# Kernel tuning notes

Hardware: AMD Instinct MI355X
Metric: run time of the kernel (lower is better)

The kernel has to match this reference:

```python
import jax, jax.numpy as jnp
import numpy as np

T, B, IN_S, H, OUT_S = 2048, 4096, 1, 20, 1


def setup_inputs() -> dict:
    key = jax.random.key(0)
    k_u, k_ih, k_hh, k_out = jax.random.split(key, 4)
    s = 1.0 / np.sqrt(H)  # PyTorch-style uniform init scale (values only; math identical)
    return {
        "u": jax.random.normal(k_u, (T, B, IN_S), dtype=jnp.float32),
        "W_ih": jax.random.uniform(k_ih, (4 * H, IN_S), minval=-s, maxval=s, dtype=jnp.float32),
        "W_hh": jax.random.uniform(k_hh, (4 * H, H), minval=-s, maxval=s, dtype=jnp.float32),
        "W_out": jax.random.uniform(k_out, (OUT_S, H), minval=-s, maxval=s, dtype=jnp.float32),
    }


def _lstm(u, W_ih, W_hh):
    # u: [T, B, IN_S]; PyTorch gate order: i, f, g, o. No biases (bias=False).
    Tn, Bn, _ = u.shape
    # Precompute input projections for all timesteps at once: [T, B, 4H]
    x_proj = jnp.einsum("tbi,gi->tbg", u, W_ih)

    def step(carry, xg):
        h, c = carry  # [B, H] each
        gates = xg + h @ W_hh.T  # [B, 4H]
        i, f, g, o = jnp.split(gates, 4, axis=-1)
        i = jax.nn.sigmoid(i)
        f = jax.nn.sigmoid(f)
        g = jnp.tanh(g)
        o = jax.nn.sigmoid(o)
        c = f * c + i * g
        h = o * jnp.tanh(c)
        return (h, c), h

    h0 = jnp.zeros((Bn, W_hh.shape[1]), dtype=u.dtype)
    c0 = jnp.zeros_like(h0)
    (_, _), ys = jax.lax.scan(step, (h0, c0), x_proj)
    return ys  # [T, B, H]


def reference(u, W_ih, W_hh, W_out):
    ys = _lstm(u, W_ih, W_hh)          # [T, B, H]
    return jnp.einsum("tbh,oh->tbo", ys, W_out)  # [T, B, OUT_S]
```

## Files before the change

kernel.cpp:

```cpp
#include <hip/hip_runtime.h>
#include <hip/hip_bf16.h>
#include <math.h>

#define TT 2048
#define BB 4096
#define HH 20

typedef float v2f __attribute__((ext_vector_type(2)));

#define L2E 1.4426950408889634f

__device__ __forceinline__ float rcp_fast(float x)  { return __builtin_amdgcn_rcpf(x); }
__device__ __forceinline__ float exp2_fast(float x) { return __builtin_amdgcn_exp2f(x); }

__device__ __forceinline__ v2f pk_fma(v2f a, v2f b, v2f c) {
    return __builtin_elementwise_fma(a, b, c);
}

__global__ __launch_bounds__(64, 2) void lstm_fused_kernel(
    const float* __restrict__ u,
    const float* __restrict__ W_ih,
    const float* __restrict__ W_hh,
    const float* __restrict__ W_out,
    float* __restrict__ y)
{
    __shared__ __align__(16) float hbuf[4][HH];

    const int lane  = threadIdx.x;
    const int group = lane / HH;
    const int j     = lane - group * HH;
    const bool is_y = (lane >= 2 * HH) && (lane < 2 * HH + 2);
    const int b_real = blockIdx.x * 2 + group;
    const bool active = (group < 2) && (b_real < BB);
    const int b = active ? b_real : 0;

    for (int i = lane; i < 4 * HH; i += 64) ((float*)hbuf)[i] = 0.0f;
    asm volatile("" ::: "memory");

    v2f wg[4][HH / 2];
    const float gsc[4] = {-L2E, -L2E, -2.0f * L2E, -L2E};
    #pragma unroll
    for (int g = 0; g < 4; ++g) {
        #pragma unroll
        for (int m = 0; m < HH / 2; ++m) {
            wg[g][m].x = gsc[g] * W_hh[(g * HH + j) * HH + 2 * m];
            wg[g][m].y = gsc[g] * W_hh[(g * HH + j) * HH + 2 * m + 1];
        }
    }
    v2f wih2[4];
    #pragma unroll
    for (int g = 0; g < 4; ++g) { wih2[g].x = gsc[g] * W_ih[g * HH + j]; wih2[g].y = 0.0f; }

    int bg = group;
    if (lane >= 2 * HH) {
        bg = is_y ? (lane - 2 * HH) : 2;
        if (is_y) {
            #pragma unroll
            for (int m = 0; m < HH / 2; ++m) {
                wg[0][m].x = W_out[2 * m];
                wg[0][m].y = W_out[2 * m + 1];
            }
            wih2[0].x = 0.0f;
        }
    }

    #pragma unroll
    for (int g = 0; g < 4; ++g) {
        #pragma unroll
        for (int m = 0; m < HH / 2; ++m) {
            asm volatile("" : "+v"(wg[g][m].x), "+v"(wg[g][m].y));
        }
        asm volatile("" : "+v"(wih2[g].x));
    }

    const v2f* hs = (const v2f*)(&hbuf[bg][0]);

    float c = 0.0f;
    const float* __restrict__ up = u + b;
    float* yp = y + blockIdx.x * 2 + (lane - 2 * HH);

    float u_cur[8];
    #pragma unroll
    for (int k = 0; k < 8; ++k) u_cur[k] = up[(size_t)k * BB];

    for (int t8 = 0; t8 < TT; t8 += 8) {
        const int tn = (t8 + 8 < TT) ? (t8 + 8) : t8;
        float u_nxt[8];
        #pragma unroll
        for (int k = 0; k < 8; ++k) u_nxt[k] = up[(size_t)(tn + k) * BB];

        float y8[8];

        #pragma unroll
        for (int tt = 0; tt < 8; ++tt) {
            v2f h2[10];
            #pragma unroll
            for (int m = 0; m < 10; ++m) h2[m] = hs[m];

            const float uv = u_cur[tt];
            const v2f uv2 = {uv, uv};
            v2f a0 = wih2[0] * uv2;
            v2f a1 = wih2[1] * uv2;
            v2f a2 = wih2[2] * uv2;
            v2f a3 = wih2[3] * uv2;

            #pragma unroll
            for (int m = 0; m < 10; ++m) {
                v2f hp = h2[m];
                a2 = pk_fma(wg[2][m], hp, a2);
                a1 = pk_fma(wg[1][m], hp, a1);
                a0 = pk_fma(wg[0][m], hp, a0);
                a3 = pk_fma(wg[3][m], hp, a3);
            }
            const float g2 = a2.x + a2.y;
            const float g1 = a1.x + a1.y;
            const float g0 = a0.x + a0.y;
            const float g3 = a3.x + a3.y;
            y8[tt] = g0;

            const float eg = exp2_fast(g2);
            const float ef = exp2_fast(g1);
            const float ei = exp2_fast(g0);
            const float eo = exp2_fast(g3);
            const float pg  = 1.0f + eg;
            const float pf  = 1.0f + ef;
            const float pi_ = 1.0f + ei;
            const float po  = 1.0f + eo;
            const float mg  = 1.0f - eg;

            const float m1  = pg * pi_;
            const float num = fmaf(c, m1, mg * pf);
            const float r   = rcp_fast(pf * m1);
            c = num * r;
            const float kn  = (-2.0f * L2E) * fabsf(num);
            const float ec  = exp2_fast(kn * r);
            const float pc  = 1.0f + ec;
            const float mcs = copysignf(1.0f - ec, num);
            const float h   = mcs * rcp_fast(po * pc);

            hbuf[group][j] = h;
        }

        if (is_y) {
            #pragma unroll
            for (int k = 0; k < 8; ++k) {
                const int idx = t8 - 1 + k;
                if (idx >= 0) yp[(size_t)idx * BB] = y8[k];
            }
        }

        #pragma unroll
        for (int k = 0; k < 8; ++k) u_cur[k] = u_nxt[k];
    }

    {
        v2f ay = {0.0f, 0.0f};
        #pragma unroll
        for (int m = 0; m < 10; ++m) ay = pk_fma(wg[0][m], hs[m], ay);
        if (is_y) yp[(size_t)(TT - 1) * BB] = ay.x + ay.y;
    }
}

extern "C" void kernel_launch(void* const* d_in, const int* in_sizes, int n_in,
                              void* d_out, int out_size, void* d_ws, size_t ws_size,
                              hipStream_t stream) {
    const float* u     = (const float*)d_in[0];
    const float* W_ih  = (const float*)d_in[1];
    const float* W_hh  = (const float*)d_in[2];
    const float* W_out = (const float*)d_in[3];
    float* y = (float*)d_out;

    const int blocks = BB / 2;
    lstm_fused_kernel<<<dim3(blocks), dim3(64), 0, stream>>>(u, W_ih, W_hh, W_out, y);
}
```

Before: 803.9 us.

## Compute two hidden units per lane to pack four batch rows per wave

Each lane now owns two hidden units of one batch element, so a 64-lane wave handles four sequences instead of two and the grid halves. Gate math and the cell update are written on 2-wide vectors, and the hidden state is stored as a pair. Holding twice as many weights in registers forces one wave per SIMD, which trades latency hiding for fewer waves and better lane utilization.

```diff
diff --git a/kernel.cpp b/kernel.cpp
--- a/kernel.cpp
+++ b/kernel.cpp
@@ -16,72 +16,90 @@
 __device__ __forceinline__ v2f pk_fma(v2f a, v2f b, v2f c) {
     return __builtin_elementwise_fma(a, b, c);
 }
+__device__ __forceinline__ v2f exp2v(v2f x) { v2f r; r.x = exp2_fast(x.x); r.y = exp2_fast(x.y); return r; }
+__device__ __forceinline__ v2f rcpv(v2f x)  { v2f r; r.x = rcp_fast(x.x);  r.y = rcp_fast(x.y);  return r; }
+__device__ __forceinline__ v2f absv(v2f x)  { v2f r; r.x = fabsf(x.x);     r.y = fabsf(x.y);     return r; }
+__device__ __forceinline__ v2f csignv(v2f x, v2f s) {
+    v2f r; r.x = copysignf(x.x, s.x); r.y = copysignf(x.y, s.y); return r;
+}
 
-__global__ __launch_bounds__(64, 2) void lstm_fused_kernel(
+__global__ __launch_bounds__(64, 1) void lstm_fused_kernel(
     const float* __restrict__ u,
     const float* __restrict__ W_ih,
     const float* __restrict__ W_hh,
     const float* __restrict__ W_out,
     float* __restrict__ y)
 {
-    __shared__ __align__(16) float hbuf[4][HH];
+    __shared__ __align__(16) float hbuf[128];
 
-    const int lane  = threadIdx.x;
-    const int group = lane / HH;
-    const int j     = lane - group * HH;
-    const bool is_y = (lane >= 2 * HH) && (lane < 2 * HH + 2);
-    const int b_real = blockIdx.x * 2 + group;
-    const bool active = (group < 2) && (b_real < BB);
-    const int b = active ? b_real : 0;
+    const int lane = threadIdx.x;
+    int q, wa, jbase;
+    bool is_y = false;
+    if (lane < 40) {
+        q = lane / 10;
+        const int p = lane - q * 10;
+        wa = q * HH + 2 * p;
+        jbase = 2 * p;
+    } else {
+        is_y = (lane < 44);
+        q = is_y ? (lane - 40) : 0;
+        wa = 4 * HH + (lane - 40) * 2;
+        jbase = 0;
+    }
 
-    for (int i = lane; i < 4 * HH; i += 64) ((float*)hbuf)[i] = 0.0f;
+    for (int i = lane; i < 128; i += 64) hbuf[i] = 0.0f;
     asm volatile("" ::: "memory");
 
-    v2f wg[4][HH / 2];
+    v2f wgv[4][2][10];
+    v2f wihv[4][2];
     const float gsc[4] = {-L2E, -L2E, -2.0f * L2E, -L2E};
     #pragma unroll
     for (int g = 0; g < 4; ++g) {
         #pragma unroll
-        for (int m = 0; m < HH / 2; ++m) {
-            wg[g][m].x = gsc[g] * W_hh[(g * HH + j) * HH + 2 * m];
-            wg[g][m].y = gsc[g] * W_hh[(g * HH + j) * HH + 2 * m + 1];
+        for (int r = 0; r < 2; ++r) {
+            const int row = g * HH + jbase + r;
+            #pragma unroll
+            for (int m = 0; m < 10; ++m) {
+                wgv[g][r][m].x = gsc[g] * W_hh[row * HH + 2 * m];
+                wgv[g][r][m].y = gsc[g] * W_hh[row * HH + 2 * m + 1];
+            }
+            wihv[g][r].x = gsc[g] * W_ih[row];
+            wihv[g][r].y = 0.0f;
         }
     }
-    v2f wih2[4];
-    #pragma unroll
-    for (int g = 0; g < 4; ++g) { wih2[g].x = gsc[g] * W_ih[g * HH + j]; wih2[g].y = 0.0f; }
-
-    int bg = group;
-    if (lane >= 2 * HH) {
-        bg = is_y ? (lane - 2 * HH) : 2;
-        if (is_y) {
-            #pragma unroll
-            for (int m = 0; m < HH / 2; ++m) {
-                wg[0][m].x = W_out[2 * m];
-                wg[0][m].y = W_out[2 * m + 1];
-            }
-            wih2[0].x = 0.0f;
+    if (lane >= 40) {
+        #pragma unroll
+        for (int m = 0; m < 10; ++m) {
+            wgv[0][0][m].x = W_out[2 * m];
+            wgv[0][0][m].y = W_out[2 * m + 1];
         }
+        wihv[0][0].x = 0.0f;
     }
 
     #pragma unroll
     for (int g = 0; g < 4; ++g) {
         #pragma unroll
-        for (int m = 0; m < HH / 2; ++m) {
-            asm volatile("" : "+v"(wg[g][m].x), "+v"(wg[g][m].y));
+        for (int r = 0; r < 2; ++r) {
+            #pragma unroll
+            for (int m = 0; m < 10; ++m)
+                asm volatile("" : "+v"(wgv[g][r][m].x), "+v"(wgv[g][r][m].y));
+            asm volatile("" : "+v"(wihv[g][r].x));
         }
-        asm volatile("" : "+v"(wih2[g].x));
     }
 
-    const v2f* hs = (const v2f*)(&hbuf[bg][0]);
+    const v2f* hs = (const v2f*)&hbuf[q * HH];
+    v2f* hw = (v2f*)&hbuf[wa];
 
-    float c = 0.0f;
-    const float* __restrict__ up = u + b;
-    float* yp = y + blockIdx.x * 2 + (lane - 2 * HH);
+    v2f cv = {0.0f, 0.0f};
+    const float* __restrict__ up = u + (size_t)blockIdx.x * 4 + q;
+    float* yp = y + (size_t)blockIdx.x * 4 + (lane - 40);
 
     float u_cur[8];
     #pragma unroll
     for (int k = 0; k < 8; ++k) u_cur[k] = up[(size_t)k * BB];
+
+    const v2f one = {1.0f, 1.0f};
+    const v2f n2l2e = {-2.0f * L2E, -2.0f * L2E};
 
     for (int t8 = 0; t8 < TT; t8 += 8) {
         const int tn = (t8 + 8 < TT) ? (t8 + 8) : t8;
@@ -99,46 +117,50 @@
 
             const float uv = u_cur[tt];
             const v2f uv2 = {uv, uv};
-            v2f a0 = wih2[0] * uv2;
-            v2f a1 = wih2[1] * uv2;
-            v2f a2 = wih2[2] * uv2;
-            v2f a3 = wih2[3] * uv2;
+            v2f a[4][2];
+            #pragma unroll
+            for (int g = 0; g < 4; ++g) {
+                #pragma unroll
+                for (int r = 0; r < 2; ++r) a[g][r] = wihv[g][r] * uv2;
+            }
 
             #pragma unroll
             for (int m = 0; m < 10; ++m) {
-                v2f hp = h2[m];
-                a2 = pk_fma(wg[2][m], hp, a2);
-                a1 = pk_fma(wg[1][m], hp, a1);
-                a0 = pk_fma(wg[0][m], hp, a0);
-                a3 = pk_fma(wg[3][m], hp, a3);
+                const v2f hp = h2[m];
+                a[2][0] = pk_fma(wgv[2][0][m], hp, a[2][0]);
+                a[2][1] = pk_fma(wgv[2][1][m], hp, a[2][1]);
+                a[1][0] = pk_fma(wgv[1][0][m], hp, a[1][0]);
+                a[1][1] = pk_fma(wgv[1][1][m], hp, a[1][1]);
+                a[0][0] = pk_fma(wgv[0][0][m], hp, a[0][0]);
+                a[0][1] = pk_fma(wgv[0][1][m], hp, a[0][1]);
+                a[3][0] = pk_fma(wgv[3][0][m], hp, a[3][0]);
+                a[3][1] = pk_fma(wgv[3][1][m], hp, a[3][1]);
             }
-            const float g2 = a2.x + a2.y;
-            const float g1 = a1.x + a1.y;
-            const float g0 = a0.x + a0.y;
-            const float g3 = a3.x + a3.y;
-            y8[tt] = g0;
+            v2f gi, gf, gg, go;
+            gi.x = a[0][0].x + a[0][0].y;  gi.y = a[0][1].x + a[0][1].y;
+            gf.x = a[1][0].x + a[1][0].y;  gf.y = a[1][1].x + a[1][1].y;
+            gg.x = a[2][0].x + a[2][0].y;  gg.y = a[2][1].x + a[2][1].y;
+            go.x = a[3][0].x + a[3][0].y;  go.y = a[3][1].x + a[3][1].y;
+            y8[tt] = gi.x;
 
-            const float eg = exp2_fast(g2);
-            const float ef = exp2_fast(g1);
-            const float ei = exp2_fast(g0);
-            const float eo = exp2_fast(g3);
-            const float pg  = 1.0f + eg;
-            const float pf  = 1.0f + ef;
-            const float pi_ = 1.0f + ei;
-            const float po  = 1.0f + eo;
-            const float mg  = 1.0f - eg;
+            const v2f eg = exp2v(gg);
+            const v2f ef = exp2v(gf);
+            const v2f ei = exp2v(gi);
+            const v2f eo = exp2v(go);
+            const v2f pg = one + eg, pf = one + ef, pi2 = one + ei, po = one + eo;
+            const v2f mg = one - eg;
 
-            const float m1  = pg * pi_;
-            const float num = fmaf(c, m1, mg * pf);
-            const float r   = rcp_fast(pf * m1);
-            c = num * r;
-            const float kn  = (-2.0f * L2E) * fabsf(num);
-            const float ec  = exp2_fast(kn * r);
-            const float pc  = 1.0f + ec;
-            const float mcs = copysignf(1.0f - ec, num);
-            const float h   = mcs * rcp_fast(po * pc);
+            const v2f m1  = pg * pi2;
+            const v2f num = pk_fma(cv, m1, mg * pf);
+            const v2f rv  = rcpv(pf * m1);
+            cv = num * rv;
+            const v2f kn  = absv(num) * n2l2e;
+            const v2f ec  = exp2v(kn * rv);
+            const v2f pc  = one + ec;
+            const v2f mcs = csignv(one - ec, num);
+            const v2f hv  = mcs * rcpv(po * pc);
 
-            hbuf[group][j] = h;
+            *hw = hv;
         }
 
         if (is_y) {
@@ -156,7 +178,7 @@
     {
         v2f ay = {0.0f, 0.0f};
         #pragma unroll
-        for (int m = 0; m < 10; ++m) ay = pk_fma(wg[0][m], hs[m], ay);
+        for (int m = 0; m < 10; ++m) ay = pk_fma(wgv[0][0][m], hs[m], ay);
         if (is_y) yp[(size_t)(TT - 1) * BB] = ay.x + ay.y;
     }
 }
@@ -170,6 +192,6 @@
     const float* W_out = (const float*)d_in[3];
     float* y = (float*)d_out;
 
-    const int blocks = BB / 2;
+    const int blocks = BB / 4;
     lstm_fused_kernel<<<dim3(blocks), dim3(64), 0, stream>>>(u, W_ih, W_hh, W_out, y);
 }
```

New measurement: 752.1 us. -6.4%, faster.
